# Kernel optimization log

Measured on AMD Instinct MI355X. Metric: run time of the kernel, lower is better.

Reference implementation:

```python
import jax, jax.numpy as jnp
import numpy as np

B, C, H, W = 8, 256, 64, 64
CQ = C // 8  # q/k projection dim = 32


def setup_inputs() -> dict:
    key = jax.random.key(0)
    ks = jax.random.split(key, 8)
    sq = 1.0 / np.sqrt(C)
    return {
        "x": jax.random.normal(ks[0], (B, C, H, W), dtype=jnp.float32),
        "wq": jax.random.normal(ks[1], (CQ, C), dtype=jnp.float32) * sq,
        "bq": jax.random.normal(ks[2], (CQ,), dtype=jnp.float32) * 0.01,
        "wk": jax.random.normal(ks[3], (CQ, C), dtype=jnp.float32) * sq,
        "bk": jax.random.normal(ks[4], (CQ,), dtype=jnp.float32) * 0.01,
        "wv": jax.random.normal(ks[5], (C, C), dtype=jnp.float32) * sq,
        "bv": jax.random.normal(ks[6], (C,), dtype=jnp.float32) * 0.01,
        "gamma": jax.random.normal(ks[7], (1,), dtype=jnp.float32) * 0.1,
    }


def reference(x, wq, bq, wk, bk, wv, bv, gamma):
    b, c, h, w = x.shape
    n = h * w
    xf = x.reshape(b, c, n)  # [b, C, N] (1x1 conv == channel matmul)
    q = jnp.einsum('oc,bcn->bno', wq, xf) + bq  # [b, N, Cq]
    k = jnp.einsum('oc,bcn->bon', wk, xf) + bk[None, :, None]  # [b, Cq, N]
    v = jnp.einsum('oc,bcn->bon', wv, xf) + bv[None, :, None]  # [b, C, N]
    energy = jnp.einsum('bnq,bqm->bnm', q, k)  # [b, N, N]
    attn = jax.nn.softmax(energy, axis=-1)
    # out[b,c,i] = sum_j v[b,c,j] * attn[b,i,j]  (bmm(v, attn^T))
    out = jnp.einsum('bcj,bij->bci', v, attn).reshape(b, c, h, w)
    return gamma[0] * out + x
```

## Files before the change

### kernel.cpp

```cpp
#include <hip/hip_runtime.h>
#include <hip/hip_bf16.h>
#include <stdint.h>

#define CC 256
#define CQD 32
#define NND 4096

typedef __bf16 bf16x8 __attribute__((ext_vector_type(8)));
typedef float f32x4 __attribute__((ext_vector_type(4)));

__device__ __forceinline__ bf16x8 ld_bf16x8(const __bf16* p) {
    return *reinterpret_cast<const bf16x8*>(p);
}

__global__ __launch_bounds__(256) void prep_weights(
    const float* __restrict__ wq, const float* __restrict__ wk,
    const float* __restrict__ wv, __bf16* __restrict__ wqkb,
    __bf16* __restrict__ wvb) {
    int i = blockIdx.x * 256 + threadIdx.x;
    if (i < 32 * 256) {
        wqkb[i] = (__bf16)wq[i];
    } else if (i < 64 * 256) {
        wqkb[i] = (__bf16)wk[i - 32 * 256];
    } else {
        int j = i - 64 * 256;
        if (j < 256 * 256) wvb[j] = (__bf16)wv[j];
    }
}

__global__ __launch_bounds__(256, 2) void proj_qkv(
    const float* __restrict__ x, const __bf16* __restrict__ wqkb,
    const __bf16* __restrict__ wvb, const float* __restrict__ bq,
    const float* __restrict__ bk, const float* __restrict__ bv,
    __bf16* __restrict__ qb, __bf16* __restrict__ kb,
    __bf16* __restrict__ vb) {
    __shared__ __align__(16) __bf16 xt[64 * 256];

    const int blk = blockIdx.x;
    const int b = blk & 7;
    const int n0 = (blk >> 3) * 64;
    const int tid = threadIdx.x;

    {
        const int tx = tid & 63;
        const int ty = tid >> 6;
        const float* xcol = x + (size_t)b * CC * NND + n0 + tx;
#pragma unroll
        for (int it = 0; it < 8; it++) {
            int c8 = it * 4 + ty;
            int c = c8 * 8;
            union { bf16x8 v; __bf16 h[8]; } pk;
#pragma unroll
            for (int u = 0; u < 8; u++)
                pk.h[u] = (__bf16)xcol[(size_t)(c + u) * NND];
            *reinterpret_cast<bf16x8*>(&xt[tx * 256 + ((c8 ^ (tx & 7)) * 8)]) = pk.v;
        }
    }
    __syncthreads();

    const int lane = tid & 63;
    const int w = tid >> 6;
    const int l15 = lane & 15;
    const int quad = lane >> 4;
    const int row = w * 16 + l15;
    const int n = n0 + row;
    const f32x4 fzero = {0.f, 0.f, 0.f, 0.f};
    f32x4 aqk[4];
    f32x4 av[16];
#pragma unroll
    for (int i = 0; i < 4; i++) aqk[i] = fzero;
#pragma unroll
    for (int i = 0; i < 16; i++) av[i] = fzero;
#pragma unroll
    for (int k0 = 0; k0 < CC; k0 += 32) {
        int g = (k0 >> 3) + quad;
        bf16x8 bf = ld_bf16x8(&xt[row * 256 + ((g ^ (row & 7)) * 8)]);
#pragma unroll
        for (int mt = 0; mt < 4; mt++) {
            bf16x8 af = ld_bf16x8(wqkb + (size_t)(mt * 16 + l15) * CC + k0 + quad * 8);
            aqk[mt] = __builtin_amdgcn_mfma_f32_16x16x32_bf16(af, bf, aqk[mt], 0, 0, 0);
        }
#pragma unroll
        for (int mt = 0; mt < 16; mt++) {
            bf16x8 af = ld_bf16x8(wvb + (size_t)(mt * 16 + l15) * CC + k0 + quad * 8);
            av[mt] = __builtin_amdgcn_mfma_f32_16x16x32_bf16(af, bf, av[mt], 0, 0, 0);
        }
    }
#pragma unroll
    for (int mt = 0; mt < 4; mt++) {
        const int ob = (mt & 1) * 16 + quad * 4;
        const float* bias = (mt < 2) ? bq : bk;
        __bf16* dst = ((mt < 2) ? qb : kb) + ((size_t)b * NND + n) * CQD + ob;
        union { ushort4 u; __bf16 h[4]; } pk;
#pragma unroll
        for (int r = 0; r < 4; r++) pk.h[r] = (__bf16)(aqk[mt][r] + bias[ob + r]);
        *reinterpret_cast<ushort4*>(dst) = pk.u;
    }
#pragma unroll
    for (int mt = 0; mt < 16; mt++) {
#pragma unroll
        for (int r = 0; r < 4; r++) {
            int c = mt * 16 + quad * 4 + r;
            vb[((size_t)b * CC + c) * NND + n] = (__bf16)(av[mt][r] + bv[c]);
        }
    }
}

__global__ __launch_bounds__(256, 2) void attention(
    const __bf16* __restrict__ qb, const __bf16* __restrict__ kb,
    const __bf16* __restrict__ vb, const float* __restrict__ gamma,
    const float* __restrict__ x, float* __restrict__ out) {
    __shared__ __align__(16) __bf16 Vt[CC * 64];
    __shared__ __align__(16) __bf16 Pt[64 * 72];
    __shared__ float aL[64];
    __shared__ float lL[64];

    const int blk = blockIdx.x;
    const int b = blk & 7;
    const int i0 = (blk >> 3) * 64;
    const int tid = threadIdx.x;
    const int w = tid >> 6;
    const int lane = tid & 63;
    const int l15 = lane & 15;
    const int quad = lane >> 4;
    const f32x4 fzero = {0.f, 0.f, 0.f, 0.f};

    bf16x8 qf = ld_bf16x8(qb + ((size_t)b * NND + i0 + w * 16 + l15) * CQD + quad * 8);

    bf16x8 kf[4];
#pragma unroll
    for (int jt = 0; jt < 4; jt++)
        kf[jt] = ld_bf16x8(kb + ((size_t)b * NND + jt * 16 + l15) * CQD + quad * 8);

    const int vrow = lane >> 3;
    const int vswz = ((lane & 7) ^ vrow) * 8;
    const __bf16* vsrc = vb + ((size_t)(b * CC + w * 64 + vrow)) * NND + vswz;
    __bf16* vdstb = &Vt[(w * 64) * 64];

    f32x4 acc[4][4];
#pragma unroll
    for (int ct = 0; ct < 4; ct++)
#pragma unroll
        for (int it = 0; it < 4; it++) acc[ct][it] = fzero;
    float m_i = -1e30f;
    float l_i = 0.f;
    const int swz = (l15 & 7) * 8;

    for (int j0 = 0; j0 < NND; j0 += 64) {
        __syncthreads();
#pragma unroll
        for (int t = 0; t < 8; t++) {
            __builtin_amdgcn_global_load_lds(
                (const __attribute__((address_space(1))) void*)(vsrc + (size_t)t * 8 * NND + j0),
                (__attribute__((address_space(3))) void*)(vdstb + t * 8 * 64), 16, 0, 0);
        }
        f32x4 sT[4];
#pragma unroll
        for (int jt = 0; jt < 4; jt++)
            sT[jt] = __builtin_amdgcn_mfma_f32_16x16x32_bf16(kf[jt], qf, fzero, 0, 0, 0);
        if (j0 + 64 < NND) {
#pragma unroll
            for (int jt = 0; jt < 4; jt++)
                kf[jt] = ld_bf16x8(kb + ((size_t)b * NND + j0 + 64 + jt * 16 + l15) * CQD + quad * 8);
        }
        {
            float mx = -1e30f;
#pragma unroll
            for (int jt = 0; jt < 4; jt++)
#pragma unroll
                for (int r = 0; r < 4; r++) mx = fmaxf(mx, sT[jt][r]);
            mx = fmaxf(mx, __shfl_xor(mx, 16));
            mx = fmaxf(mx, __shfl_xor(mx, 32));
            float mnew = fmaxf(m_i, mx);
            float alpha = __expf(m_i - mnew);
            m_i = mnew;
            float ps = 0.f;
#pragma unroll
            for (int jt = 0; jt < 4; jt++) {
                union { ushort4 u4; __bf16 h[4]; } pk;
#pragma unroll
                for (int r = 0; r < 4; r++) {
                    float p = __expf(sT[jt][r] - mnew);
                    ps += p;
                    pk.h[r] = (__bf16)p;
                }
                *reinterpret_cast<ushort4*>(
                    &Pt[(w * 16 + l15) * 72 + jt * 16 + quad * 4]) = pk.u4;
            }
            ps += __shfl_xor(ps, 16);
            ps += __shfl_xor(ps, 32);
            l_i = l_i * alpha + ps;
            if (quad == 0) aL[w * 16 + l15] = alpha;
        }
        __syncthreads();
        float av[4];
#pragma unroll
        for (int it = 0; it < 4; it++) av[it] = aL[it * 16 + l15];
#pragma unroll
        for (int ct = 0; ct < 4; ct++)
#pragma unroll
            for (int it = 0; it < 4; it++) acc[ct][it] *= av[it];
#pragma unroll
        for (int ks = 0; ks < 2; ks++) {
            bf16x8 vf[4];
#pragma unroll
            for (int ct = 0; ct < 4; ct++) {
                int cr = w * 64 + ct * 16 + l15;
                vf[ct] = ld_bf16x8(&Vt[cr * 64 + ((ks * 32 + quad * 8) ^ swz)]);
            }
#pragma unroll
            for (int it = 0; it < 4; it++) {
                bf16x8 pf = ld_bf16x8(&Pt[(it * 16 + l15) * 72 + ks * 32 + quad * 8]);
#pragma unroll
                for (int ct = 0; ct < 4; ct++)
                    acc[ct][it] = __builtin_amdgcn_mfma_f32_16x16x32_bf16(vf[ct], pf, acc[ct][it], 0, 0, 0);
            }
        }
    }
    __syncthreads();
    if (quad == 0) lL[w * 16 + l15] = l_i;
    __syncthreads();
    float linv[4];
#pragma unroll
    for (int it = 0; it < 4; it++) linv[it] = 1.0f / lL[it * 16 + l15];
    float g = gamma[0];
#pragma unroll
    for (int ct = 0; ct < 4; ct++) {
#pragma unroll
        for (int it = 0; it < 4; it++) {
#pragma unroll
            for (int r = 0; r < 4; r++) {
                int c = w * 64 + ct * 16 + quad * 4 + r;
                int i = i0 + it * 16 + l15;
                size_t off = ((size_t)b * CC + c) * NND + i;
                out[off] = g * (acc[ct][it][r] * linv[it]) + x[off];
            }
        }
    }
}

extern "C" void kernel_launch(void* const* d_in, const int* in_sizes, int n_in,
                              void* d_out, int out_size, void* d_ws, size_t ws_size,
                              hipStream_t stream) {
    const float* x = (const float*)d_in[0];
    const float* wq = (const float*)d_in[1];
    const float* bq = (const float*)d_in[2];
    const float* wk = (const float*)d_in[3];
    const float* bk = (const float*)d_in[4];
    const float* wv = (const float*)d_in[5];
    const float* bv = (const float*)d_in[6];
    const float* gamma = (const float*)d_in[7];
    float* out = (float*)d_out;

    char* ws = (char*)d_ws;
    __bf16* qb = (__bf16*)ws;
    __bf16* kb = (__bf16*)(ws + 2097152);
    __bf16* vb = (__bf16*)(ws + 2 * 2097152);
    __bf16* wqkb = (__bf16*)(ws + 2 * 2097152 + 16777216);
    __bf16* wvb = (__bf16*)(ws + 2 * 2097152 + 16777216 + 32768);

    prep_weights<<<320, 256, 0, stream>>>(wq, wk, wv, wqkb, wvb);
    proj_qkv<<<512, 256, 0, stream>>>(x, wqkb, wvb, bq, bk, bv, qb, kb, vb);
    attention<<<512, 256, 0, stream>>>(qb, kb, vb, gamma, x, out);
}
```

Before: 242.3 us.

## Load V fragments directly into registers and double-buffer P to drop a barrier

```diff
diff --git a/kernel.cpp b/kernel.cpp
--- a/kernel.cpp
+++ b/kernel.cpp
@@ -110,9 +110,8 @@
     const __bf16* __restrict__ qb, const __bf16* __restrict__ kb,
     const __bf16* __restrict__ vb, const float* __restrict__ gamma,
     const float* __restrict__ x, float* __restrict__ out) {
-    __shared__ __align__(16) __bf16 Vt[CC * 64];
-    __shared__ __align__(16) __bf16 Pt[64 * 72];
-    __shared__ float aL[64];
+    __shared__ __align__(16) __bf16 Pt[2][64 * 72];
+    __shared__ float aL[2][64];
     __shared__ float lL[64];
 
     const int blk = blockIdx.x;
@@ -125,17 +124,10 @@
     const int quad = lane >> 4;
     const f32x4 fzero = {0.f, 0.f, 0.f, 0.f};
 
-    bf16x8 qf = ld_bf16x8(qb + ((size_t)b * NND + i0 + w * 16 + l15) * CQD + quad * 8);
-
-    bf16x8 kf[4];
-#pragma unroll
-    for (int jt = 0; jt < 4; jt++)
-        kf[jt] = ld_bf16x8(kb + ((size_t)b * NND + jt * 16 + l15) * CQD + quad * 8);
-
-    const int vrow = lane >> 3;
-    const int vswz = ((lane & 7) ^ vrow) * 8;
-    const __bf16* vsrc = vb + ((size_t)(b * CC + w * 64 + vrow)) * NND + vswz;
-    __bf16* vdstb = &Vt[(w * 64) * 64];
+    const bf16x8 qf = ld_bf16x8(qb + ((size_t)b * NND + i0 + w * 16 + l15) * CQD + quad * 8);
+
+    const __bf16* kbase = kb + (size_t)b * NND * CQD + l15 * CQD + quad * 8;
+    const __bf16* vbase = vb + ((size_t)(b * CC + w * 64 + l15)) * NND + quad * 8;
 
     f32x4 acc[4][4];
 #pragma unroll
@@ -144,16 +136,20 @@
         for (int it = 0; it < 4; it++) acc[ct][it] = fzero;
     float m_i = -1e30f;
     float l_i = 0.f;
-    const int swz = (l15 & 7) * 8;
+
+    bf16x8 kf[4];
+#pragma unroll
+    for (int jt = 0; jt < 4; jt++)
+        kf[jt] = ld_bf16x8(kbase + (size_t)jt * 16 * CQD);
 
     for (int j0 = 0; j0 < NND; j0 += 64) {
-        __syncthreads();
-#pragma unroll
-        for (int t = 0; t < 8; t++) {
-            __builtin_amdgcn_global_load_lds(
-                (const __attribute__((address_space(1))) void*)(vsrc + (size_t)t * 8 * NND + j0),
-                (__attribute__((address_space(3))) void*)(vdstb + t * 8 * 64), 16, 0, 0);
-        }
+        const int pb = (j0 >> 6) & 1;
+        bf16x8 vf[8];
+#pragma unroll
+        for (int ks = 0; ks < 2; ks++)
+#pragma unroll
+            for (int ct = 0; ct < 4; ct++)
+                vf[ks * 4 + ct] = ld_bf16x8(vbase + (size_t)ct * 16 * NND + j0 + ks * 32);
         f32x4 sT[4];
 #pragma unroll
         for (int jt = 0; jt < 4; jt++)
@@ -161,7 +157,7 @@
         if (j0 + 64 < NND) {
 #pragma unroll
             for (int jt = 0; jt < 4; jt++)
-                kf[jt] = ld_bf16x8(kb + ((size_t)b * NND + j0 + 64 + jt * 16 + l15) * CQD + quad * 8);
+                kf[jt] = ld_bf16x8(kbase + (size_t)(j0 + 64 + jt * 16) * CQD);
         }
         {
             float mx = -1e30f;
@@ -185,39 +181,34 @@
                     pk.h[r] = (__bf16)p;
                 }
                 *reinterpret_cast<ushort4*>(
-                    &Pt[(w * 16 + l15) * 72 + jt * 16 + quad * 4]) = pk.u4;
+                    &Pt[pb][(w * 16 + l15) * 72 + jt * 16 + quad * 4]) = pk.u4;
             }
             ps += __shfl_xor(ps, 16);
             ps += __shfl_xor(ps, 32);
             l_i = l_i * alpha + ps;
-            if (quad == 0) aL[w * 16 + l15] = alpha;
+            if (quad == 0) aL[pb][w * 16 + l15] = alpha;
         }
         __syncthreads();
-        float av[4];
-#pragma unroll
-        for (int it = 0; it < 4; it++) av[it] = aL[it * 16 + l15];
+        float avs[4];
+#pragma unroll
+        for (int it = 0; it < 4; it++) avs[it] = aL[pb][it * 16 + l15];
 #pragma unroll
         for (int ct = 0; ct < 4; ct++)
 #pragma unroll
-            for (int it = 0; it < 4; it++) acc[ct][it] *= av[it];
+            for (int it = 0; it < 4; it++) acc[ct][it] *= avs[it];
 #pragma unroll
         for (int ks = 0; ks < 2; ks++) {
-            bf16x8 vf[4];
-#pragma unroll
-            for (int ct = 0; ct < 4; ct++) {
-                int cr = w * 64 + ct * 16 + l15;
-                vf[ct] = ld_bf16x8(&Vt[cr * 64 + ((ks * 32 + quad * 8) ^ swz)]);
+#pragma unroll
+            for (int it = 0; it < 4; it++) {
+                bf16x8 pf = ld_bf16x8(&Pt[pb][(it * 16 + l15) * 72 + ks * 32 + quad * 8]);
+#pragma unroll
+                for (int ct = 0; ct < 4; ct++)
+                    acc[ct][it] = __builtin_amdgcn_mfma_f32_16x16x32_bf16(
+                        vf[ks * 4 + ct], pf, acc[ct][it], 0, 0, 0);
             }
-#pragma unroll
-            for (int it = 0; it < 4; it++) {
-                bf16x8 pf = ld_bf16x8(&Pt[(it * 16 + l15) * 72 + ks * 32 + quad * 8]);
-#pragma unroll
-                for (int ct = 0; ct < 4; ct++)
-                    acc[ct][it] = __builtin_amdgcn_mfma_f32_16x16x32_bf16(vf[ct], pf, acc[ct][it], 0, 0, 0);
-            }
-        }
-    }
-    __syncthreads();
+        }
+    }
+
     if (quad == 0) lL[w * 16 + l15] = l_i;
     __syncthreads();
     float linv[4];
```

After: 283.4 us. 1.17x slower.

## Replace online softmax max with Cauchy-Schwarz static bound and exp2 scaling

Applied to the files above, without the earlier changes.

```diff
diff --git a/kernel.cpp b/kernel.cpp
--- a/kernel.cpp
+++ b/kernel.cpp
@@ -5,6 +5,7 @@
 #define CC 256
 #define CQD 32
 #define NND 4096
+#define LOG2E 1.44269504f
 
 typedef __bf16 bf16x8 __attribute__((ext_vector_type(8)));
 typedef float f32x4 __attribute__((ext_vector_type(4)));
@@ -19,7 +20,7 @@
     __bf16* __restrict__ wvb) {
     int i = blockIdx.x * 256 + threadIdx.x;
     if (i < 32 * 256) {
-        wqkb[i] = (__bf16)wq[i];
+        wqkb[i] = (__bf16)(wq[i] * LOG2E);
     } else if (i < 64 * 256) {
         wqkb[i] = (__bf16)wk[i - 32 * 256];
     } else {
@@ -33,7 +34,7 @@
     const __bf16* __restrict__ wvb, const float* __restrict__ bq,
     const float* __restrict__ bk, const float* __restrict__ bv,
     __bf16* __restrict__ qb, __bf16* __restrict__ kb,
-    __bf16* __restrict__ vb) {
+    __bf16* __restrict__ vb, float* __restrict__ kmax) {
     __shared__ __align__(16) __bf16 xt[64 * 256];
 
     const int blk = blockIdx.x;
@@ -86,15 +87,30 @@
             av[mt] = __builtin_amdgcn_mfma_f32_16x16x32_bf16(af, bf, av[mt], 0, 0, 0);
         }
     }
+    float kss = 0.f;
 #pragma unroll
     for (int mt = 0; mt < 4; mt++) {
         const int ob = (mt & 1) * 16 + quad * 4;
-        const float* bias = (mt < 2) ? bq : bk;
         __bf16* dst = ((mt < 2) ? qb : kb) + ((size_t)b * NND + n) * CQD + ob;
         union { ushort4 u; __bf16 h[4]; } pk;
 #pragma unroll
-        for (int r = 0; r < 4; r++) pk.h[r] = (__bf16)(aqk[mt][r] + bias[ob + r]);
+        for (int r = 0; r < 4; r++) {
+            float bias = (mt < 2) ? bq[ob + r] * LOG2E : bk[ob + r];
+            float v = aqk[mt][r] + bias;
+            if (mt >= 2) kss += v * v;
+            pk.h[r] = (__bf16)v;
+        }
         *reinterpret_cast<ushort4*>(dst) = pk.u;
+    }
+    kss += __shfl_xor(kss, 16);
+    kss += __shfl_xor(kss, 32);
+    kss = fmaxf(kss, __shfl_xor(kss, 1));
+    kss = fmaxf(kss, __shfl_xor(kss, 2));
+    kss = fmaxf(kss, __shfl_xor(kss, 4));
+    kss = fmaxf(kss, __shfl_xor(kss, 8));
+    if (lane == 0) {
+        kss *= 1.04f;
+        atomicMax((unsigned int*)&kmax[b], __float_as_uint(kss));
     }
 #pragma unroll
     for (int mt = 0; mt < 16; mt++) {
@@ -108,11 +124,11 @@
 
 __global__ __launch_bounds__(256, 2) void attention(
     const __bf16* __restrict__ qb, const __bf16* __restrict__ kb,
-    const __bf16* __restrict__ vb, const float* __restrict__ gamma,
-    const float* __restrict__ x, float* __restrict__ out) {
+    const __bf16* __restrict__ vb, const float* __restrict__ kmax,
+    const float* __restrict__ gamma, const float* __restrict__ x,
+    float* __restrict__ out) {
     __shared__ __align__(16) __bf16 Vt[CC * 64];
     __shared__ __align__(16) __bf16 Pt[64 * 72];
-    __shared__ float aL[64];
     __shared__ float lL[64];
 
     const int blk = blockIdx.x;
@@ -127,6 +143,16 @@
 
     bf16x8 qf = ld_bf16x8(qb + ((size_t)b * NND + i0 + w * 16 + l15) * CQD + quad * 8);
 
+    float q2 = 0.f;
+#pragma unroll
+    for (int u = 0; u < 8; u++) {
+        float v = (float)qf[u];
+        q2 += v * v;
+    }
+    q2 += __shfl_xor(q2, 16);
+    q2 += __shfl_xor(q2, 32);
+    const float m_s = sqrtf(q2 * kmax[b]);
+
     bf16x8 kf[4];
 #pragma unroll
     for (int jt = 0; jt < 4; jt++)
@@ -142,7 +168,6 @@
     for (int ct = 0; ct < 4; ct++)
 #pragma unroll
         for (int it = 0; it < 4; it++) acc[ct][it] = fzero;
-    float m_i = -1e30f;
     float l_i = 0.f;
     const int swz = (l15 & 7) * 8;
 
@@ -164,42 +189,22 @@
                 kf[jt] = ld_bf16x8(kb + ((size_t)b * NND + j0 + 64 + jt * 16 + l15) * CQD + quad * 8);
         }
         {
-            float mx = -1e30f;
-#pragma unroll
-            for (int jt = 0; jt < 4; jt++)
-#pragma unroll
-                for (int r = 0; r < 4; r++) mx = fmaxf(mx, sT[jt][r]);
-            mx = fmaxf(mx, __shfl_xor(mx, 16));
-            mx = fmaxf(mx, __shfl_xor(mx, 32));
-            float mnew = fmaxf(m_i, mx);
-            float alpha = __expf(m_i - mnew);
-            m_i = mnew;
             float ps = 0.f;
 #pragma unroll
             for (int jt = 0; jt < 4; jt++) {
                 union { ushort4 u4; __bf16 h[4]; } pk;
 #pragma unroll
                 for (int r = 0; r < 4; r++) {
-                    float p = __expf(sT[jt][r] - mnew);
+                    float p = exp2f(sT[jt][r] - m_s);
                     ps += p;
                     pk.h[r] = (__bf16)p;
                 }
                 *reinterpret_cast<ushort4*>(
                     &Pt[(w * 16 + l15) * 72 + jt * 16 + quad * 4]) = pk.u4;
             }
-            ps += __shfl_xor(ps, 16);
-            ps += __shfl_xor(ps, 32);
-            l_i = l_i * alpha + ps;
-            if (quad == 0) aL[w * 16 + l15] = alpha;
+            l_i += ps;
         }
         __syncthreads();
-        float av[4];
-#pragma unroll
-        for (int it = 0; it < 4; it++) av[it] = aL[it * 16 + l15];
-#pragma unroll
-        for (int ct = 0; ct < 4; ct++)
-#pragma unroll
-            for (int it = 0; it < 4; it++) acc[ct][it] *= av[it];
 #pragma unroll
         for (int ks = 0; ks < 2; ks++) {
             bf16x8 vf[4];
@@ -218,6 +223,8 @@
         }
     }
     __syncthreads();
+    l_i += __shfl_xor(l_i, 16);
+    l_i += __shfl_xor(l_i, 32);
     if (quad == 0) lL[w * 16 + l15] = l_i;
     __syncthreads();
     float linv[4];
@@ -258,8 +265,10 @@
     __bf16* vb = (__bf16*)(ws + 2 * 2097152);
     __bf16* wqkb = (__bf16*)(ws + 2 * 2097152 + 16777216);
     __bf16* wvb = (__bf16*)(ws + 2 * 2097152 + 16777216 + 32768);
-
+    float* kmaxb = (float*)(ws + 2 * 2097152 + 16777216 + 32768 + 131072);
+
+    hipMemsetAsync(kmaxb, 0, 8 * sizeof(float), stream);
     prep_weights<<<320, 256, 0, stream>>>(wq, wk, wv, wqkb, wvb);
-    proj_qkv<<<512, 256, 0, stream>>>(x, wqkb, wvb, bq, bk, bv, qb, kb, vb);
-    attention<<<512, 256, 0, stream>>>(qb, kb, vb, gamma, x, out);
-}
+    proj_qkv<<<512, 256, 0, stream>>>(x, wqkb, wvb, bq, bk, bv, qb, kb, vb, kmaxb);
+    attention<<<512, 256, 0, stream>>>(qb, kb, vb, kmaxb, gamma, x, out);
+}
```

Measured after the change: 267.6 us. 10.4% more time.
